# Optimization experiments

Measured on AMD Instinct MI355X. Metric: run time of the kernel, lower is better.

Reference implementation:

```python
import jax, jax.numpy as jnp
import numpy as np

B, NPG, K, C, IN_DIM, GS_DIM, NBLK, NCLF = 8, 12500, 128, 128, 7, 11, 4, 5
N = B * NPG          # 100000 total nodes
E = N * 8            # 800000 nnz in block-diagonal complex gradient operator


def setup_inputs() -> dict:
    key = jax.random.key(0)
    ks = jax.random.split(key, 20)
    x = jax.random.normal(ks[0], (N, IN_DIM), jnp.float32)
    evals = jax.random.uniform(ks[1], (B, K), jnp.float32) * 10.0  # nonneg eigenvalues
    evecs = jax.random.normal(ks[2], (N, K), jnp.float32) / np.float32(np.sqrt(NPG))
    mass = jax.random.uniform(ks[3], (N,), jnp.float32) + 0.1      # positive lumped mass
    graph_stats = jax.random.normal(ks[4], (B, GS_DIM), jnp.float32)
    batch = jnp.repeat(jnp.arange(B, dtype=jnp.int32), NPG)        # sorted graph ids
    epg = E // B
    offs = jnp.repeat(jnp.arange(B, dtype=jnp.int32) * NPG, epg)   # block-diagonal structure
    grad_rows = jax.random.randint(ks[5], (E,), 0, NPG, jnp.int32) + offs
    grad_cols = jax.random.randint(ks[6], (E,), 0, NPG, jnp.int32) + offs
    grad_vals_re = jax.random.normal(ks[7], (E,), jnp.float32) * 0.1
    grad_vals_im = jax.random.normal(ks[8], (E,), jnp.float32) * 0.1
    grad_n = jnp.full((B,), NPG, jnp.int32)
    s = lambda k, sh, fan: jax.random.normal(k, sh, jnp.float32) / np.float32(np.sqrt(fan))
    W_embed = s(ks[9], (IN_DIM, C), IN_DIM); b_embed = jnp.zeros((C,), jnp.float32)
    t_diff = jax.random.uniform(ks[10], (NBLK, C), jnp.float32) * 0.5 + 1e-3
    A_grad = s(ks[11], (NBLK, C, C), C)
    W1 = s(ks[12], (NBLK, 3 * C, C), 3 * C); b1 = jnp.zeros((NBLK, C), jnp.float32)
    W2 = s(ks[13], (NBLK, C, C), C);         b2 = jnp.zeros((NBLK, C), jnp.float32)
    Wh1 = s(ks[14], (C + GS_DIM, 64), C + GS_DIM); bh1 = jnp.zeros((64,), jnp.float32)
    Wh2 = s(ks[15], (64, NCLF), 64);               bh2 = jnp.zeros((NCLF,), jnp.float32)
    return dict(x=x, evals=evals, evecs=evecs, mass=mass, graph_stats=graph_stats,
                batch=batch, grad_rows=grad_rows, grad_cols=grad_cols,
                grad_vals_re=grad_vals_re, grad_vals_im=grad_vals_im, grad_n=grad_n,
                W_embed=W_embed, b_embed=b_embed, t_diff=t_diff, A_grad=A_grad,
                W1=W1, b1=b1, W2=W2, b2=b2, Wh1=Wh1, bh1=bh1, Wh2=Wh2, bh2=bh2)


def _forward(x, evals, evecs, mass, graph_stats, batch, grad_rows, grad_cols,
             vre, vim, W_embed, b_embed, t_diff, A_grad, W1, b1, W2, b2,
             Wh1, bh1, Wh2, bh2):
    n = x.shape[0]
    ev_r = evecs.reshape(B, NPG, K)              # per-graph spectral basis (equal-size graphs)
    h = jax.nn.relu(x @ W_embed + b_embed)       # embed: [N, C]
    for blk in range(NBLK):                      # fixed small number of blocks
        # --- learned-time spectral diffusion ---
        time = jnp.clip(jnp.abs(t_diff[blk]), 1e-8)            # [C]
        hm = (h * mass[:, None]).reshape(B, NPG, C)
        spec = jnp.einsum('bnk,bnc->bkc', ev_r, hm)            # to_basis: [B, K, C]
        spec = spec * jnp.exp(-evals[:, :, None] * time[None, None, :])
        h_diff = jnp.einsum('bnk,bkc->bnc', ev_r, spec).reshape(n, C)
        # --- block-sparse complex gradient: g = (vre + i*vim) @ h_diff ---
        xg = h_diff[grad_cols]                                 # [E, C] gather
        g_re = jnp.zeros((n, C), h.dtype).at[grad_rows].add(vre[:, None] * xg)
        g_im = jnp.zeros((n, C), h.dtype).at[grad_rows].add(vim[:, None] * xg)
        # --- spatial gradient features: tanh(Re(conj(g) * (A g))) ---
        A = A_grad[blk]
        g_feat = jnp.tanh(g_re * (g_re @ A.T) + g_im * (g_im @ A.T))
        # --- per-vertex MLP + residual (dropout = eval-mode identity) ---
        comb = jnp.concatenate([h, h_diff, g_feat], axis=-1)   # [N, 3C]
        h = h + (jax.nn.relu(comb @ W1[blk] + b1[blk]) @ W2[blk] + b2[blk])
    # --- fuse per-node features with gathered graph stats, node clf head ---
    fused = jnp.concatenate([h, graph_stats[batch]], axis=-1)  # [N, C+11]
    return jax.nn.relu(fused @ Wh1 + bh1) @ Wh2 + bh2          # [N, 5]


def reference(x, evals, evecs, mass, graph_stats, batch, grad_rows, grad_cols,
              grad_vals_re, grad_vals_im, grad_n, W_embed, b_embed, t_diff,
              A_grad, W1, b1, W2, b2, Wh1, bh1, Wh2, bh2):
    # Vectorized replacement of the original per-batch .item() nnz-count loop
    # (histogram of edge rows into per-graph node-offset bins); the block-sparse
    # operator is applied directly with global COO indices so nnz is only a stat.
    node_off = jnp.concatenate([jnp.zeros((1,), jnp.int32),
                                jnp.cumsum(grad_n)[:-1].astype(jnp.int32)])
    _grad_nnz = jnp.bincount(jnp.searchsorted(node_off, grad_rows, side='right') - 1, length=B)
    return _forward(x, evals, evecs, mass, graph_stats, batch, grad_rows, grad_cols,
                    grad_vals_re, grad_vals_im, W_embed, b_embed, t_diff, A_grad,
                    W1, b1, W2, b2, Wh1, bh1, Wh2, bh2)
```

## Files before the change

kernel.cpp:

```cpp
#include <hip/hip_runtime.h>
#include <hip/hip_bf16.h>

#define NNODES 100000
#define NPG    12500
#define NGRAPH 8
#define KD     128
#define CD     128
#define INDIM  7
#define GSDIM  11
#define NBLKS  4
#define NCLF   5
#define NEDGE  800000
#define BCAP   32
#define NPGP   12800
#define TBSPLIT 40
#define TBCHUNK 320
#define NT32    391
#define NT128   98

typedef __attribute__((ext_vector_type(8))) short short8v;
typedef __attribute__((ext_vector_type(4))) float f32x4;
typedef unsigned short u16;
typedef unsigned long long u64;

#define MFMA(acc, a, b) acc = __builtin_amdgcn_mfma_f32_16x16x32_bf16(a, b, acc, 0, 0, 0)

__device__ __forceinline__ u16 f2b(float f) {
  union { __hip_bfloat16 h; u16 u; } cv;
  cv.h = __float2bfloat16(f);
  return cv.u;
}
__device__ __forceinline__ float b2f(u16 u) {
  return __uint_as_float((unsigned)u << 16);
}


__device__ __forceinline__ void stage64_f32(u16* S, const float* src, int ld, int k0, int valid) {
  int t = threadIdx.x, row = t >> 2, kq = t & 3;
  alignas(16) u16 tmp[8] = {0, 0, 0, 0, 0, 0, 0, 0};
  if (row < valid) {
    const float* p = src + (size_t)row * ld + k0 + kq * 8;
    float4 f0 = *(const float4*)p, f1 = *(const float4*)(p + 4);
    tmp[0] = f2b(f0.x); tmp[1] = f2b(f0.y); tmp[2] = f2b(f0.z); tmp[3] = f2b(f0.w);
    tmp[4] = f2b(f1.x); tmp[5] = f2b(f1.y); tmp[6] = f2b(f1.z); tmp[7] = f2b(f1.w);
  }
  *(uint4*)&S[row * 40 + kq * 8] = *(uint4*)tmp;
}

__device__ __forceinline__ void stage64_b16(u16* S, const u16* src, long ld, int k0, int valid) {
  int t = threadIdx.x, row = t >> 2, kq = t & 3;
  uint4 v = make_uint4(0, 0, 0, 0);
  if (row < valid) v = *(const uint4*)(src + (size_t)row * ld + k0 + kq * 8);
  *(uint4*)&S[row * 40 + kq * 8] = v;
}

__device__ __forceinline__ void stage32_b16(u16* S, const u16* src, long ld, int k0, int valid) {
  int t = threadIdx.x;
  if (t < 128) {
    int row = t >> 2, kq = t & 3;
    uint4 v = make_uint4(0, 0, 0, 0);
    if (row < valid) v = *(const uint4*)(src + (size_t)row * ld + k0 + kq * 8);
    *(uint4*)&S[row * 40 + kq * 8] = v;
  }
}

__device__ __forceinline__ void stage128_b16(u16* S, const u16* src, long ld, int k0) {
  int t = threadIdx.x, row = t >> 1, half = t & 1;
  const u16* p = src + (size_t)row * ld + k0 + half * 16;
  uint4 v0 = *(const uint4*)p, v1 = *(const uint4*)(p + 8);
  *(uint4*)&S[row * 40 + half * 16] = v0;
  *(uint4*)&S[row * 40 + half * 16 + 8] = v1;
}

__device__ __forceinline__ void stage128_f32(u16* S, const float* src, int ld, int k0) {
  int t = threadIdx.x, row = t >> 1, half = t & 1;
  const float* p = src + (size_t)row * ld + k0 + half * 16;
  float4 f0 = *(const float4*)p, f1 = *(const float4*)(p + 4);
  float4 f2 = *(const float4*)(p + 8), f3 = *(const float4*)(p + 12);
  alignas(16) u16 tmp[16];
  tmp[0] = f2b(f0.x); tmp[1] = f2b(f0.y); tmp[2]  = f2b(f0.z); tmp[3]  = f2b(f0.w);
  tmp[4] = f2b(f1.x); tmp[5] = f2b(f1.y); tmp[6]  = f2b(f1.z); tmp[7]  = f2b(f1.w);
  tmp[8] = f2b(f2.x); tmp[9] = f2b(f2.y); tmp[10] = f2b(f2.z); tmp[11] = f2b(f2.w);
  tmp[12] = f2b(f3.x); tmp[13] = f2b(f3.y); tmp[14] = f2b(f3.z); tmp[15] = f2b(f3.w);
  *(uint4*)&S[row * 40 + half * 16] = *(uint4*)&tmp[0];
  *(uint4*)&S[row * 40 + half * 16 + 8] = *(uint4*)&tmp[8];
}

__device__ __forceinline__ void stageA_b16(u16* Af, const u16* src, long ld, int valid) {
  int t = threadIdx.x;
#pragma unroll
  for (int q = 0; q < 4; ++q) {
    int lin = t + q * 512;
    int row = lin >> 4, kq = lin & 15;
    uint4 v = make_uint4(0, 0, 0, 0);
    if (row < valid) v = *(const uint4*)(src + (size_t)row * ld + kq * 8);
    *(uint4*)&Af[row * 136 + kq * 8] = v;
  }
}
__device__ __forceinline__ void stageA_f32(u16* Af, const float* src, long ld, int valid) {
  int t = threadIdx.x;
#pragma unroll
  for (int q = 0; q < 4; ++q) {
    int lin = t + q * 512;
    int row = lin >> 4, kq = lin & 15;
    alignas(16) u16 tmp[8] = {0, 0, 0, 0, 0, 0, 0, 0};
    if (row < valid) {
      const float* p = src + (size_t)row * ld + kq * 8;
      float4 f0 = *(const float4*)p, f1 = *(const float4*)(p + 4);
      tmp[0] = f2b(f0.x); tmp[1] = f2b(f0.y); tmp[2] = f2b(f0.z); tmp[3] = f2b(f0.w);
      tmp[4] = f2b(f1.x); tmp[5] = f2b(f1.y); tmp[6] = f2b(f1.z); tmp[7] = f2b(f1.w);
    }
    *(uint4*)&Af[row * 136 + kq * 8] = *(uint4*)tmp;
  }
}

__device__ __forceinline__ uint4 ldB(const u16* bt, int k0) {
  int t = threadIdx.x, row = t >> 2, kq = t & 3;
  return *(const uint4*)(bt + (size_t)row * 128 + k0 + kq * 8);
}
__device__ __forceinline__ void stB(u16* Bs, uint4 v) {
  int t = threadIdx.x, row = t >> 2, kq = t & 3;
  *(uint4*)&Bs[row * 40 + kq * 8] = v;
}

__device__ __forceinline__ short8v frag(const u16* S, int row0, int l) {
  return *(const short8v*)&S[(row0 + (l & 15)) * 40 + (l >> 4) * 8];
}
__device__ __forceinline__ short8v frag_p(const u16* S, int row0, int l, int pitch, int k0) {
  return *(const short8v*)&S[(row0 + (l & 15)) * pitch + k0 + (l >> 4) * 8];
}


__global__ void k_fill0(float4* p, int n4) {
  int i = blockIdx.x * blockDim.x + threadIdx.x;
  int s = gridDim.x * blockDim.x;
  float4 z = make_float4(0.f, 0.f, 0.f, 0.f);
  for (; i < n4; i += s) p[i] = z;
}

__global__ __launch_bounds__(256) void k_embed2(const float* __restrict__ x,
                                                const float* __restrict__ W,
                                                const float* __restrict__ bv,
                                                const float* __restrict__ mass,
                                                u16* __restrict__ h16,
                                                u16* __restrict__ hmT) {
  int b = blockIdx.x / 200, tile = blockIdx.x % 200;
  int n0 = tile * 64;
  size_t gbase = (size_t)b * NPG;
  int t = threadIdx.x;
  __shared__ float xs[64][8];
  __shared__ float Ws[INDIM][128];
  __shared__ float bs[128];
  __shared__ float ms[64];
  __shared__ float ld[64][132];
  if (t < 128) bs[t] = bv[t];
  for (int i = t; i < INDIM * 128; i += 256) Ws[i >> 7][i & 127] = W[i];
  for (int i = t; i < 64 * INDIM; i += 256) {
    int r = i / INDIM, q = i % INDIM;
    int gn = n0 + r;
    xs[r][q] = (gn < NPG) ? x[(gbase + gn) * INDIM + q] : 0.f;
  }
  if (t < 64) {
    int gn = n0 + t;
    ms[t] = (gn < NPG) ? mass[gbase + gn] : 0.f;
  }
  __syncthreads();
  {
    int row = t & 63, c0 = (t >> 6) * 32;
#pragma unroll
    for (int cc = 0; cc < 32; ++cc) {
      int c = c0 + cc;
      float acc = bs[c];
#pragma unroll
      for (int i = 0; i < INDIM; ++i) acc = fmaf(xs[row][i], Ws[i][c], acc);
      ld[row][c] = fmaxf(acc, 0.f);
    }
  }
  __syncthreads();
  {
    int row = t >> 2, q = t & 3;
    if (n0 + row < NPG) {
      size_t base = (gbase + n0 + row) * (size_t)CD + q * 32;
      alignas(16) u16 tmp[8];
#pragma unroll
      for (int u = 0; u < 4; ++u) {
#pragma unroll
        for (int i = 0; i < 8; ++i) tmp[i] = f2b(ld[row][q * 32 + u * 8 + i]);
        *(uint4*)&h16[base + u * 8] = *(uint4*)tmp;
      }
    }
  }
  {
    int crow = t >> 1, half = t & 1;
    alignas(16) u16 tmp[8];
#pragma unroll
    for (int q = 0; q < 4; ++q) {
      int nb = half * 32 + q * 8;
#pragma unroll
      for (int i = 0; i < 8; ++i) tmp[i] = f2b(ld[nb + i][crow] * ms[nb + i]);
      *(uint4*)&hmT[((size_t)(b * 128 + crow)) * NPGP + n0 + nb] = *(uint4*)tmp;
    }
  }
}

__global__ void k_bucket_place(const int* __restrict__ rows, const int* __restrict__ cols,
                               const float* __restrict__ vre, const float* __restrict__ vim,
                               int* cnt, u64* bucket) {
  int e = blockIdx.x * 256 + threadIdx.x;
  if (e >= NEDGE) return;
  int r = rows[e];
  int pos = atomicAdd(&cnt[r], 1);
  if (pos < BCAP) {
    u64 ent = (u64)(unsigned)cols[e]
            | ((u64)f2b(vre[e]) << 32)
            | ((u64)f2b(vim[e]) << 48);
    bucket[(size_t)r * BCAP + pos] = ent;
  }
}

__global__ void k_gather_ev(const int* __restrict__ cnt, const u64* __restrict__ bucket,
                            const float* __restrict__ evf, const u16* __restrict__ ev16,
                            int useB16,
                            u16* __restrict__ gre, u16* __restrict__ gim) {
  int orig = blockIdx.x;
  int blk  = (orig & 7) * 3125 + (orig >> 3);
  int wv = threadIdx.x >> 6;
  int ln = threadIdx.x & 63;
  int r  = blk * 4 + wv;
  int d = min(cnt[r], BCAP);
  const u64* bk = bucket + (size_t)r * BCAP;
  float2 ra0 = make_float2(0.f, 0.f), ia0 = make_float2(0.f, 0.f);
  float2 ra1 = make_float2(0.f, 0.f), ia1 = make_float2(0.f, 0.f);
  if (useB16) {
    int i = 0;
    for (; i + 2 <= d; i += 2) {
      u64 e0 = bk[i], e1 = bk[i + 1];
      int c0 = (int)(unsigned)e0, c1 = (int)(unsigned)e1;
      float a0 = b2f((u16)(e0 >> 32)), b0 = b2f((u16)(e0 >> 48));
      float a1 = b2f((u16)(e1 >> 32)), b1 = b2f((u16)(e1 >> 48));
      ushort2 u0 = *(const ushort2*)&ev16[(size_t)c0 * KD + ln * 2];
      ushort2 u1 = *(const ushort2*)&ev16[(size_t)c1 * KD + ln * 2];
      float vx0 = b2f(u0.x), vy0 = b2f(u0.y);
      float vx1 = b2f(u1.x), vy1 = b2f(u1.y);
      ra0.x = fmaf(a0, vx0, ra0.x); ra0.y = fmaf(a0, vy0, ra0.y);
      ia0.x = fmaf(b0, vx0, ia0.x); ia0.y = fmaf(b0, vy0, ia0.y);
      ra1.x = fmaf(a1, vx1, ra1.x); ra1.y = fmaf(a1, vy1, ra1.y);
      ia1.x = fmaf(b1, vx1, ia1.x); ia1.y = fmaf(b1, vy1, ia1.y);
    }
    if (i < d) {
      u64 e0 = bk[i];
      int c0 = (int)(unsigned)e0;
      float a0 = b2f((u16)(e0 >> 32)), b0 = b2f((u16)(e0 >> 48));
      ushort2 u0 = *(const ushort2*)&ev16[(size_t)c0 * KD + ln * 2];
      float vx0 = b2f(u0.x), vy0 = b2f(u0.y);
      ra0.x = fmaf(a0, vx0, ra0.x); ra0.y = fmaf(a0, vy0, ra0.y);
      ia0.x = fmaf(b0, vx0, ia0.x); ia0.y = fmaf(b0, vy0, ia0.y);
    }
  } else {
    for (int i = 0; i < d; ++i) {
      u64 e0 = bk[i];
      int c0 = (int)(unsigned)e0;
      float a = b2f((u16)(e0 >> 32)), b = b2f((u16)(e0 >> 48));
      float2 v = *(const float2*)&evf[(size_t)c0 * KD + ln * 2];
      ra0.x = fmaf(a, v.x, ra0.x); ra0.y = fmaf(a, v.y, ra0.y);
      ia0.x = fmaf(b, v.x, ia0.x); ia0.y = fmaf(b, v.y, ia0.y);
    }
  }
  ushort2 ro, io;
  ro.x = f2b(ra0.x + ra1.x); ro.y = f2b(ra0.y + ra1.y);
  io.x = f2b(ia0.x + ia1.x); io.y = f2b(ia0.y + ia1.y);
  *(ushort2*)&gre[(size_t)r * KD + ln * 2] = ro;
  *(ushort2*)&gim[(size_t)r * KD + ln * 2] = io;
}

__global__ void k_prep_w(const float* __restrict__ W1, const float* __restrict__ W2,
                         u16* W1aT, u16* W1bT, u16* W1cT, u16* W2T) {
  int idx = blockIdx.x * 256 + threadIdx.x;
  int blk = idx >> 16, rem = idx & 65535;
  int mat = rem >> 14, e = rem & 16383;
  int j = e >> 7, c = e & 127;
  float v;
  u16* dst;
  if (mat < 3) {
    v = W1[(size_t)blk * 3 * 16384 + (size_t)mat * 16384 + e];
    dst = (mat == 0) ? W1aT : (mat == 1 ? W1bT : W1cT);
  } else {
    v = W2[(size_t)blk * 16384 + e];
    dst = W2T;
  }
  dst[(size_t)blk * 16384 + c * 128 + j] = f2b(v);
}

__global__ void k_prep_head(const float* __restrict__ Wh1, const float* __restrict__ Wh2,
                            u16* __restrict__ B1T, u16* __restrict__ B2T) {
  for (int idx = threadIdx.x; idx < 64 * 160; idx += 256) {
    int c = idx / 160, k = idx % 160;
    B1T[idx] = f2b(k < (CD + GSDIM) ? Wh1[k * 64 + c] : 0.f);
  }
  for (int idx = threadIdx.x; idx < 16 * 64; idx += 256) {
    int c = idx >> 6, k = idx & 63;
    B2T[idx] = f2b(c < NCLF ? Wh2[k * NCLF + c] : 0.f);
  }
}

__global__ void k_transpose_nk(const float* __restrict__ src, u16* __restrict__ dst,
                               u16* __restrict__ ev16, int writeMir) {
  int b = blockIdx.x / 200, tile = blockIdx.x % 200;
  int n0 = tile * 64;
  size_t gbase = (size_t)b * NPG;
  int t = threadIdx.x;
  __shared__ float ld[64][132];
  int row0 = t >> 5, c4 = t & 31;
#pragma unroll
  for (int it = 0; it < 8; ++it) {
    int r = it * 8 + row0;
    int gn = n0 + r;
    float4 v = make_float4(0.f, 0.f, 0.f, 0.f);
    if (gn < NPG) v = *(const float4*)&src[(gbase + gn) * KD + c4 * 4];
    *(float4*)&ld[r][c4 * 4] = v;
    if (writeMir && gn < NPG) {
      ushort4 o;
      o.x = f2b(v.x); o.y = f2b(v.y); o.z = f2b(v.z); o.w = f2b(v.w);
      *(ushort4*)&ev16[(gbase + gn) * KD + c4 * 4] = o;
    }
  }
  __syncthreads();
  int crow = t >> 1, half = t & 1;
  alignas(16) u16 tmp[8];
#pragma unroll
  for (int q = 0; q < 4; ++q) {
    int nb = half * 32 + q * 8;
#pragma unroll
    for (int i = 0; i < 8; ++i) tmp[i] = f2b(ld[nb + i][crow]);
    *(uint4*)&dst[((size_t)(b * 128 + crow)) * NPGP + n0 + nb] = *(uint4*)tmp;
  }
}


__global__ __launch_bounds__(256) void k_tobasis(const u16* __restrict__ evT,
                                                 const u16* __restrict__ hmT,
                                                 float* __restrict__ partials) {
  int g = blockIdx.x;
  int kt = g & 1;
  int s  = (g >> 1) % TBSPLIT;
  int b  = g / (2 * TBSPLIT);
  int t = threadIdx.x, w = t >> 6, l = t & 63;
  __shared__ u16 As[64 * 40];
  __shared__ u16 Bs[128 * 40];
  f32x4 acc[8];
  f32x4 z = {0.f, 0.f, 0.f, 0.f};
#pragma unroll
  for (int j = 0; j < 8; ++j) acc[j] = z;
  const u16* ae = evT + ((size_t)(b * 128 + kt * 64)) * NPGP + s * TBCHUNK;
  const u16* bh = hmT + (size_t)b * 128 * NPGP + s * TBCHUNK;
  for (int ks = 0; ks < TBCHUNK / 32; ++ks) {
    stage64_b16(As, ae, NPGP, ks * 32, 64);
    stage128_b16(Bs, bh, NPGP, ks * 32);
    __syncthreads();
    short8v a = frag(As, w * 16, l);
    __builtin_amdgcn_s_setprio(1);
#pragma unroll
    for (int j = 0; j < 8; ++j) MFMA(acc[j], a, frag(Bs, j * 16, l));
    __builtin_amdgcn_s_setprio(0);
    __syncthreads();
  }
  float* op = partials + (size_t)(b * TBSPLIT + s) * 16384 + kt * 64 * 128;
#pragma unroll
  for (int j = 0; j < 8; ++j)
#pragma unroll
    for (int i = 0; i < 4; ++i) {
      int krow = w * 16 + (l >> 4) * 4 + i;
      int c = j * 16 + (l & 15);
      op[krow * 128 + c] = acc[j][i];
    }
}

__global__ void k_reduce_scale_t(const float* __restrict__ partials,
                                 const float* __restrict__ evals,
                                 const float* __restrict__ td,
                                 float* __restrict__ spec, u16* __restrict__ specT) {
  int b = blockIdx.x >> 6;
  int idx = (blockIdx.x & 63) * 256 + threadIdx.x;
  int k = idx >> 7, c = idx & 127;
  float s = 0.f;
#pragma unroll 8
  for (int sp = 0; sp < TBSPLIT; ++sp)
    s += partials[(size_t)(b * TBSPLIT + sp) * 16384 + idx];
  float tm = fmaxf(fabsf(td[c]), 1e-8f);
  s *= expf(-evals[b * KD + k] * tm);
  spec[(size_t)b * 16384 + idx] = s;
  specT[(size_t)b * 16384 + c * 128 + k] = f2b(s);
}

__global__ __launch_bounds__(256) void k_smallT(const float* __restrict__ Agrad_blk,
                                                const u16* __restrict__ W1bT_blk,
                                                const float* __restrict__ spec,
                                                u16* __restrict__ SAT, u16* __restrict__ M1T) {
  int b = blockIdx.x & 7;
  int job = (blockIdx.x >> 3) & 1;
  int q = blockIdx.x >> 4;
  int t = threadIdx.x, w = t >> 6, l = t & 63;
  __shared__ u16 As[128 * 40];
  __shared__ u16 Bs[128 * 40];
  f32x4 acc[2][2];
  f32x4 z = {0.f, 0.f, 0.f, 0.f};
#pragma unroll
  for (int mi = 0; mi < 2; ++mi) { acc[mi][0] = z; acc[mi][1] = z; }
  for (int ks = 0; ks < 4; ++ks) {
    if (job == 0) stage128_f32(As, Agrad_blk, 128, ks * 32);
    else          stage128_b16(As, W1bT_blk, 128, ks * 32);
    stage128_f32(Bs, spec + (size_t)b * 16384, 128, ks * 32);
    __syncthreads();
    short8v a0 = frag(As, q * 32, l);
    short8v a1 = frag(As, q * 32 + 16, l);
#pragma unroll
    for (int jj = 0; jj < 2; ++jj) {
      short8v bj = frag(Bs, (w * 2 + jj) * 16, l);
      MFMA(acc[0][jj], a0, bj);
      MFMA(acc[1][jj], a1, bj);
    }
    __syncthreads();
  }
  u16* out = (job == 0 ? SAT : M1T) + (size_t)b * 16384;
#pragma unroll
  for (int mi = 0; mi < 2; ++mi)
#pragma unroll
    for (int jj = 0; jj < 2; ++jj)
#pragma unroll
      for (int i = 0; i < 4; ++i)
        out[(q * 32 + mi * 16 + (l >> 4) * 4 + i) * 128 + (w * 2 + jj) * 16 + (l & 15)] =
            f2b(acc[mi][jj][i]);
}

__global__ __launch_bounds__(256) void k_gfeat(const u16* __restrict__ Gre,
                                               const u16* __restrict__ Gim,
                                               const u16* __restrict__ specT,
                                               const u16* __restrict__ SAT,
                                               u16* __restrict__ gf) {
  int b = blockIdx.x / NT32, tile = blockIdx.x % NT32;
  int n0 = tile * 32;
  size_t gbase = (size_t)b * NPG;
  int t = threadIdx.x, w = t >> 6, l = t & 63;
  int r0 = (w & 1) * 16, c0 = (w >> 1) * 64;
  __shared__ u16 Sr[32 * 40];
  __shared__ u16 Si[32 * 40];
  __shared__ u16 Bs[128 * 40];
  __shared__ u16 Ba[128 * 40];
  f32x4 aGR[4], aAR[4], aGI[4], aAI[4];
  f32x4 z = {0.f, 0.f, 0.f, 0.f};
#pragma unroll
  for (int j = 0; j < 4; ++j) { aGR[j] = z; aAR[j] = z; aGI[j] = z; aAI[j] = z; }
  int valid = min(32, NPG - n0);
  const u16* gre = Gre + (gbase + n0) * KD;
  const u16* gim = Gim + (gbase + n0) * KD;
  for (int ks = 0; ks < 4; ++ks) {
    stage32_b16(Sr, gre, KD, ks * 32, valid);
    stage32_b16(Si, gim, KD, ks * 32, valid);
    stage128_b16(Bs, specT + (size_t)b * 16384, 128, ks * 32);
    stage128_b16(Ba, SAT + (size_t)b * 16384, 128, ks * 32);
    __syncthreads();
    short8v fr = frag(Sr, r0, l);
    short8v fi = frag(Si, r0, l);
    __builtin_amdgcn_s_setprio(1);
#pragma unroll
    for (int j = 0; j < 4; ++j) {
      short8v bs = frag(Bs, c0 + j * 16, l);
      short8v ba = frag(Ba, c0 + j * 16, l);
      MFMA(aGR[j], fr, bs);
      MFMA(aAR[j], fr, ba);
      MFMA(aGI[j], fi, bs);
      MFMA(aAI[j], fi, ba);
    }
    __builtin_amdgcn_s_setprio(0);
    __syncthreads();
  }
#pragma unroll
  for (int j = 0; j < 4; ++j) {
    int c = c0 + j * 16 + (l & 15);
#pragma unroll
    for (int i = 0; i < 4; ++i) {
      int n = n0 + r0 + (l >> 4) * 4 + i;
      if (n - n0 < valid) {
        float v = tanhf(fmaf(aGR[j][i], aAR[j][i], aGI[j][i] * aAI[j][i]));
        gf[(gbase + n) * CD + c] = f2b(v);
      }
    }
  }
}

__global__ __launch_bounds__(512) void k_mlp12(const float* __restrict__ evf,
                                               const u16* __restrict__ ev16,
                                               int useB16,
                                               const u16* __restrict__ gf,
                                               const u16* __restrict__ W1aT,
                                               const u16* __restrict__ M1T,
                                               const u16* __restrict__ W1cT,
                                               const float* __restrict__ b1,
                                               const u16* __restrict__ W2T,
                                               const float* __restrict__ b2,
                                               const float* __restrict__ mass,
                                               u16* __restrict__ h16,
                                               u16* __restrict__ hmT,
                                               int writeHmT) {
  int b = blockIdx.x / NT128, tile = blockIdx.x % NT128;
  int n0 = tile * 128;
  size_t gbase = (size_t)b * NPG;
  int t = threadIdx.x, w = t >> 6, l = t & 63;
  __shared__ u16 SH[27648];
  u16* Af  = SH;
  u16* t1S = SH;
  u16* Tm  = SH;
  u16* Bs0 = SH + 17408;
  u16* Bs1 = SH + 22528;
  f32x4 acc[8];
  f32x4 z = {0.f, 0.f, 0.f, 0.f};
#pragma unroll
  for (int j = 0; j < 8; ++j) acc[j] = z;
  int valid = min(128, NPG - n0);
  int r0 = w * 16;

  for (int seg = 0; seg < 3; ++seg) {
    const u16* bt = (seg == 0) ? W1aT : (seg == 1 ? M1T + (size_t)b * 16384 : W1cT);
    if (seg == 0)      stageA_b16(Af, h16 + (gbase + n0) * CD, CD, valid);
    else if (seg == 1) {
      if (useB16) stageA_b16(Af, ev16 + (gbase + n0) * KD, KD, valid);
      else        stageA_f32(Af, evf + (gbase + n0) * KD, KD, valid);
    }
    else               stageA_b16(Af, gf + (gbase + n0) * CD, CD, valid);
    stB(Bs0, ldB(bt, 0));
    __syncthreads();
#pragma unroll
    for (int ks = 0; ks < 4; ++ks) {
      uint4 bvn;
      if (ks < 3) bvn = ldB(bt, (ks + 1) * 32);
      short8v a = frag_p(Af, r0, l, 136, ks * 32);
      u16* Bcur = (ks & 1) ? Bs1 : Bs0;
      __builtin_amdgcn_s_setprio(1);
#pragma unroll
      for (int j = 0; j < 8; ++j) MFMA(acc[j], a, frag(Bcur, j * 16, l));
      __builtin_amdgcn_s_setprio(0);
      if (ks < 3) stB((ks & 1) ? Bs0 : Bs1, bvn);
      __syncthreads();
    }
  }
#pragma unroll
  for (int j = 0; j < 8; ++j) {
    int c = j * 16 + (l & 15);
    float bias = b1[c];
#pragma unroll
    for (int i = 0; i < 4; ++i) {
      int row = r0 + (l >> 4) * 4 + i;
      t1S[row * 132 + c] = f2b(fmaxf(acc[j][i] + bias, 0.f));
    }
  }
  stB(Bs0, ldB(W2T, 0));
  __syncthreads();

#pragma unroll
  for (int j = 0; j < 8; ++j) acc[j] = z;
#pragma unroll
  for (int ks = 0; ks < 4; ++ks) {
    uint4 bvn;
    if (ks < 3) bvn = ldB(W2T, (ks + 1) * 32);
    short8v a = frag_p(t1S, r0, l, 132, ks * 32);
    u16* Bcur = (ks & 1) ? Bs1 : Bs0;
    __builtin_amdgcn_s_setprio(1);
#pragma unroll
    for (int j = 0; j < 8; ++j) MFMA(acc[j], a, frag(Bcur, j * 16, l));
    __builtin_amdgcn_s_setprio(0);
    if (ks < 3) stB((ks & 1) ? Bs0 : Bs1, bvn);
    __syncthreads();
  }

  float massv[4];
#pragma unroll
  for (int i = 0; i < 4; ++i) {
    int nl = r0 + (l >> 4) * 4 + i;
    massv[i] = (nl < valid) ? mass[gbase + n0 + nl] : 0.f;
  }
#pragma unroll
  for (int j = 0; j < 8; ++j) {
    int c = j * 16 + (l & 15);
    float bias = b2[c];
#pragma unroll
    for (int i = 0; i < 4; ++i) {
      int nl = r0 + (l >> 4) * 4 + i;
      float hv = 0.f;
      if (nl < valid) {
        size_t idx = (gbase + n0 + nl) * (size_t)CD + c;
        hv = b2f(h16[idx]) + acc[j][i] + bias;
        h16[idx] = f2b(hv);
      }
      if (writeHmT) Tm[c * 130 + nl] = f2b(hv * massv[i]);
    }
  }
  if (writeHmT) {
    __syncthreads();
#pragma unroll
    for (int q = 0; q < 4; ++q) {
      int lin = t + q * 512;
      int cc = lin >> 4, chunk = lin & 15;
      *(uint4*)&hmT[((size_t)(b * 128 + cc)) * NPGP + n0 + chunk * 8] =
          *(const uint4*)&Tm[cc * 130 + chunk * 8];
    }
  }
}

__global__ __launch_bounds__(256) void k_head2(
    const u16* __restrict__ h16, const float* __restrict__ gs,
    const int* __restrict__ batch, const u16* __restrict__ B1T,
    const float* __restrict__ bh1, const u16* __restrict__ B2T,
    const float* __restrict__ bh2, float* __restrict__ out) {
  int n0 = blockIdx.x * 64;
  int t = threadIdx.x, w = t >> 6, l = t & 63;
  __shared__ u16 As[64 * 40];
  __shared__ u16 Bs[64 * 40];
  __shared__ u16 zS[64 * 72];
  int valid = min(64, NNODES - n0);
  f32x4 acc1[4];
  f32x4 z = {0.f, 0.f, 0.f, 0.f};
#pragma unroll
  for (int j = 0; j < 4; ++j) acc1[j] = z;
  for (int ks = 0; ks < 5; ++ks) {
    if (ks < 4) {
      stage64_b16(As, h16 + (size_t)n0 * CD, CD, ks * 32, valid);
    } else {
      int row = t >> 2, kq = t & 3;
      alignas(16) u16 tmp[8];
      int bb = (row < valid) ? batch[n0 + row] : 0;
#pragma unroll
      for (int q = 0; q < 8; ++q) {
        int kk = kq * 8 + q;
        float v = (row < valid && kk < GSDIM) ? gs[bb * GSDIM + kk] : 0.f;
        tmp[q] = f2b(v);
      }
      *(uint4*)&As[row * 40 + kq * 8] = *(uint4*)tmp;
    }
    stage64_b16(Bs, B1T, 160, ks * 32, 64);
    __syncthreads();
    short8v a = frag(As, w * 16, l);
#pragma unroll
    for (int j = 0; j < 4; ++j) MFMA(acc1[j], a, frag(Bs, j * 16, l));
    __syncthreads();
  }
#pragma unroll
  for (int j = 0; j < 4; ++j) {
    int c = j * 16 + (l & 15);
    float bias = bh1[c];
#pragma unroll
    for (int i = 0; i < 4; ++i) {
      int row = w * 16 + (l >> 4) * 4 + i;
      zS[row * 72 + c] = f2b(fmaxf(acc1[j][i] + bias, 0.f));
    }
  }
  __syncthreads();
  f32x4 acc2 = z;
  for (int ks = 0; ks < 2; ++ks) {
    stage64_b16(Bs, B2T, 64, ks * 32, 16);
    __syncthreads();
    short8v a2 = frag_p(zS, w * 16, l, 72, ks * 32);
    MFMA(acc2, a2, frag(Bs, 0, l));
    __syncthreads();
  }
  int c = l & 15;
  if (c < NCLF) {
    float bias = bh2[c];
#pragma unroll
    for (int i = 0; i < 4; ++i) {
      int n = n0 + w * 16 + (l >> 4) * 4 + i;
      if (n < NNODES) out[(size_t)n * NCLF + c] = acc2[i] + bias;
    }
  }
}

extern "C" void kernel_launch(void* const* d_in, const int* in_sizes, int n_in,
                              void* d_out, int out_size, void* d_ws, size_t ws_size,
                              hipStream_t stream) {
  const float* x     = (const float*)d_in[0];
  const float* evals = (const float*)d_in[1];
  const float* evecs = (const float*)d_in[2];
  const float* mass  = (const float*)d_in[3];
  const float* gs    = (const float*)d_in[4];
  const int*   batch = (const int*)d_in[5];
  const int*   grows = (const int*)d_in[6];
  const int*   gcols = (const int*)d_in[7];
  const float* vre   = (const float*)d_in[8];
  const float* vim   = (const float*)d_in[9];
  const float* Wemb  = (const float*)d_in[11];
  const float* bemb  = (const float*)d_in[12];
  const float* tdiff = (const float*)d_in[13];
  const float* Agrad = (const float*)d_in[14];
  const float* W1    = (const float*)d_in[15];
  const float* b1    = (const float*)d_in[16];
  const float* W2    = (const float*)d_in[17];
  const float* b2    = (const float*)d_in[18];
  const float* Wh1   = (const float*)d_in[19];
  const float* bh1   = (const float*)d_in[20];
  const float* Wh2   = (const float*)d_in[21];
  const float* bh2   = (const float*)d_in[22];

  char* base = (char*)d_ws;
  size_t off = 0;
  auto alloc = [&](size_t bytes) -> void* {
    void* p = base + off;
    off += (bytes + 255) & ~(size_t)255;
    return p;
  };
  u16*   evT16  = (u16*)alloc((size_t)NGRAPH * 128 * NPGP * 2);
  u16*   hmT    = (u16*)alloc((size_t)NGRAPH * 128 * NPGP * 2);
  u16*   Gre16  = (u16*)alloc((size_t)NNODES * KD * 2);
  u16*   Gim16  = (u16*)alloc((size_t)NNODES * KD * 2);
  u16*   h16    = (u16*)alloc((size_t)NNODES * CD * 2);
  float* spec   = (float*)alloc((size_t)NGRAPH * 16384 * 4);
  u16*   specT16 = (u16*)alloc((size_t)NGRAPH * 16384 * 2);
  u16*   SAT16  = (u16*)alloc((size_t)NGRAPH * 16384 * 2);
  u16*   M1T16  = (u16*)alloc((size_t)NGRAPH * 16384 * 2);
  u16*   W1aT16 = (u16*)alloc((size_t)NBLKS * 16384 * 2);
  u16*   W1bT16 = (u16*)alloc((size_t)NBLKS * 16384 * 2);
  u16*   W1cT16 = (u16*)alloc((size_t)NBLKS * 16384 * 2);
  u16*   W2T16  = (u16*)alloc((size_t)NBLKS * 16384 * 2);
  u16*   B1T16  = (u16*)alloc(64 * 160 * 2);
  u16*   B2T16  = (u16*)alloc(16 * 64 * 2);
  int*   cnt    = (int*)alloc(100352 * 4);
  void*  R      = alloc((size_t)NNODES * BCAP * 8);
  u64*   bucket = (u64*)R;
  float* partials = (float*)R;
  u16*   gf16   = (u16*)R;
  int useEv16 = 0;
  u16* ev16 = nullptr;
  if (off + ((size_t)NNODES * KD * 2 + 256) <= ws_size) {
    ev16 = (u16*)alloc((size_t)NNODES * KD * 2);
    useEv16 = 1;
  }
  float* out    = (float*)d_out;

  k_embed2<<<NGRAPH * 200, 256, 0, stream>>>(x, Wemb, bemb, mass, h16, hmT);
  k_fill0<<<98, 256, 0, stream>>>((float4*)cnt, 100352 / 4);
  k_bucket_place<<<(NEDGE + 255) / 256, 256, 0, stream>>>(grows, gcols, vre, vim,
                                                          cnt, bucket);
  k_transpose_nk<<<NGRAPH * 200, 256, 0, stream>>>(evecs, evT16, ev16, useEv16);
  k_gather_ev<<<NNODES / 4, 256, 0, stream>>>(cnt, bucket, evecs, ev16, useEv16,
                                              Gre16, Gim16);
  k_prep_w<<<1024, 256, 0, stream>>>(W1, W2, W1aT16, W1bT16, W1cT16, W2T16);
  k_prep_head<<<1, 256, 0, stream>>>(Wh1, Wh2, B1T16, B2T16);

  for (int blk = 0; blk < NBLKS; ++blk) {
    k_tobasis<<<NGRAPH * TBSPLIT * 2, 256, 0, stream>>>(evT16, hmT, partials);
    k_reduce_scale_t<<<NGRAPH * 64, 256, 0, stream>>>(partials, evals, tdiff + blk * CD,
                                                      spec, specT16);
    k_smallT<<<64, 256, 0, stream>>>(Agrad + (size_t)blk * 16384,
                                     W1bT16 + (size_t)blk * 16384, spec, SAT16, M1T16);
    k_gfeat<<<NGRAPH * NT32, 256, 0, stream>>>(Gre16, Gim16, specT16, SAT16, gf16);
    k_mlp12<<<NGRAPH * NT128, 512, 0, stream>>>(evecs, ev16, useEv16, gf16,
                                                W1aT16 + (size_t)blk * 16384, M1T16,
                                                W1cT16 + (size_t)blk * 16384,
                                                b1 + blk * CD,
                                                W2T16 + (size_t)blk * 16384,
                                                b2 + blk * CD, mass, h16, hmT,
                                                (blk < NBLKS - 1) ? 1 : 0);
  }
  k_head2<<<(NNODES + 63) / 64, 256, 0, stream>>>(h16, gs, batch, B1T16, bh1,
                                                  B2T16, bh2, out);
}
```

Measured before the change: 647.0 us.

## Fold mass into transposed evecs and compute full 128x128 tile per tobasis block

The mass weighting moves from the per-block hidden transpose (embed and mlp12 epilogues) into the one-time evecs transpose, so the hidden transpose is stored unweighted and the per-block mass loads go away. k_tobasis now computes both 64-row k halves in one workgroup with two accumulator sets, sharing each staged B tile across twice the MFMAs. The number of tobasis blocks is halved, which improves B-tile reuse at the cost of more registers per thread and fewer blocks to fill the GPU.

```diff
diff --git a/kernel.cpp b/kernel.cpp
--- a/kernel.cpp
+++ b/kernel.cpp
@@ -141,9 +141,8 @@
 __global__ __launch_bounds__(256) void k_embed2(const float* __restrict__ x,
                                                 const float* __restrict__ W,
                                                 const float* __restrict__ bv,
-                                                const float* __restrict__ mass,
                                                 u16* __restrict__ h16,
-                                                u16* __restrict__ hmT) {
+                                                u16* __restrict__ hT) {
   int b = blockIdx.x / 200, tile = blockIdx.x % 200;
   int n0 = tile * 64;
   size_t gbase = (size_t)b * NPG;
@@ -151,7 +150,6 @@
   __shared__ float xs[64][8];
   __shared__ float Ws[INDIM][128];
   __shared__ float bs[128];
-  __shared__ float ms[64];
   __shared__ float ld[64][132];
   if (t < 128) bs[t] = bv[t];
   for (int i = t; i < INDIM * 128; i += 256) Ws[i >> 7][i & 127] = W[i];
@@ -160,10 +158,6 @@
     int gn = n0 + r;
     xs[r][q] = (gn < NPG) ? x[(gbase + gn) * INDIM + q] : 0.f;
   }
-  if (t < 64) {
-    int gn = n0 + t;
-    ms[t] = (gn < NPG) ? mass[gbase + gn] : 0.f;
-  }
   __syncthreads();
   {
     int row = t & 63, c0 = (t >> 6) * 32;
@@ -197,8 +191,8 @@
     for (int q = 0; q < 4; ++q) {
       int nb = half * 32 + q * 8;
 #pragma unroll
-      for (int i = 0; i < 8; ++i) tmp[i] = f2b(ld[nb + i][crow] * ms[nb + i]);
-      *(uint4*)&hmT[((size_t)(b * 128 + crow)) * NPGP + n0 + nb] = *(uint4*)tmp;
+      for (int i = 0; i < 8; ++i) tmp[i] = f2b(ld[nb + i][crow]);
+      *(uint4*)&hT[((size_t)(b * 128 + crow)) * NPGP + n0 + nb] = *(uint4*)tmp;
     }
   }
 }
@@ -303,13 +297,18 @@
   }
 }
 
-__global__ void k_transpose_nk(const float* __restrict__ src, u16* __restrict__ dst,
-                               u16* __restrict__ ev16, int writeMir) {
+__global__ void k_transpose_nk(const float* __restrict__ src, const float* __restrict__ mass,
+                               u16* __restrict__ dst, u16* __restrict__ ev16, int writeMir) {
   int b = blockIdx.x / 200, tile = blockIdx.x % 200;
   int n0 = tile * 64;
   size_t gbase = (size_t)b * NPG;
   int t = threadIdx.x;
   __shared__ float ld[64][132];
+  __shared__ float ms[64];
+  if (t < 64) {
+    int gn = n0 + t;
+    ms[t] = (gn < NPG) ? mass[gbase + gn] : 0.f;
+  }
   int row0 = t >> 5, c4 = t & 31;
 #pragma unroll
   for (int it = 0; it < 8; ++it) {
@@ -331,48 +330,55 @@
   for (int q = 0; q < 4; ++q) {
     int nb = half * 32 + q * 8;
 #pragma unroll
-    for (int i = 0; i < 8; ++i) tmp[i] = f2b(ld[nb + i][crow]);
+    for (int i = 0; i < 8; ++i) tmp[i] = f2b(ld[nb + i][crow] * ms[nb + i]);
     *(uint4*)&dst[((size_t)(b * 128 + crow)) * NPGP + n0 + nb] = *(uint4*)tmp;
   }
 }
 
 
-__global__ __launch_bounds__(256) void k_tobasis(const u16* __restrict__ evT,
-                                                 const u16* __restrict__ hmT,
+__global__ __launch_bounds__(256) void k_tobasis(const u16* __restrict__ evTm,
+                                                 const u16* __restrict__ hT,
                                                  float* __restrict__ partials) {
-  int g = blockIdx.x;
-  int kt = g & 1;
-  int s  = (g >> 1) % TBSPLIT;
-  int b  = g / (2 * TBSPLIT);
+  int s = blockIdx.x % TBSPLIT;
+  int b = blockIdx.x / TBSPLIT;
   int t = threadIdx.x, w = t >> 6, l = t & 63;
-  __shared__ u16 As[64 * 40];
+  __shared__ u16 As[128 * 40];
   __shared__ u16 Bs[128 * 40];
-  f32x4 acc[8];
+  f32x4 acc[2][8];
   f32x4 z = {0.f, 0.f, 0.f, 0.f};
 #pragma unroll
-  for (int j = 0; j < 8; ++j) acc[j] = z;
-  const u16* ae = evT + ((size_t)(b * 128 + kt * 64)) * NPGP + s * TBCHUNK;
-  const u16* bh = hmT + (size_t)b * 128 * NPGP + s * TBCHUNK;
+  for (int mi = 0; mi < 2; ++mi)
+#pragma unroll
+    for (int j = 0; j < 8; ++j) acc[mi][j] = z;
+  const u16* ae = evTm + (size_t)b * 128 * NPGP + s * TBCHUNK;
+  const u16* bh = hT   + (size_t)b * 128 * NPGP + s * TBCHUNK;
   for (int ks = 0; ks < TBCHUNK / 32; ++ks) {
-    stage64_b16(As, ae, NPGP, ks * 32, 64);
+    stage128_b16(As, ae, NPGP, ks * 32);
     stage128_b16(Bs, bh, NPGP, ks * 32);
     __syncthreads();
-    short8v a = frag(As, w * 16, l);
+    short8v a0 = frag(As, w * 32, l);
+    short8v a1 = frag(As, w * 32 + 16, l);
     __builtin_amdgcn_s_setprio(1);
 #pragma unroll
-    for (int j = 0; j < 8; ++j) MFMA(acc[j], a, frag(Bs, j * 16, l));
+    for (int j = 0; j < 8; ++j) {
+      short8v bj = frag(Bs, j * 16, l);
+      MFMA(acc[0][j], a0, bj);
+      MFMA(acc[1][j], a1, bj);
+    }
     __builtin_amdgcn_s_setprio(0);
     __syncthreads();
   }
-  float* op = partials + (size_t)(b * TBSPLIT + s) * 16384 + kt * 64 * 128;
-#pragma unroll
-  for (int j = 0; j < 8; ++j)
-#pragma unroll
-    for (int i = 0; i < 4; ++i) {
-      int krow = w * 16 + (l >> 4) * 4 + i;
-      int c = j * 16 + (l & 15);
-      op[krow * 128 + c] = acc[j][i];
-    }
+  float* op = partials + (size_t)(b * TBSPLIT + s) * 16384;
+#pragma unroll
+  for (int mi = 0; mi < 2; ++mi)
+#pragma unroll
+    for (int j = 0; j < 8; ++j)
+#pragma unroll
+      for (int i = 0; i < 4; ++i) {
+        int krow = w * 32 + mi * 16 + (l >> 4) * 4 + i;
+        int c = j * 16 + (l & 15);
+        op[krow * 128 + c] = acc[mi][j][i];
+      }
 }
 
 __global__ void k_reduce_scale_t(const float* __restrict__ partials,
@@ -498,10 +504,9 @@
                                                const float* __restrict__ b1,
                                                const u16* __restrict__ W2T,
                                                const float* __restrict__ b2,
-                                               const float* __restrict__ mass,
                                                u16* __restrict__ h16,
-                                               u16* __restrict__ hmT,
-                                               int writeHmT) {
+                                               u16* __restrict__ hT,
+                                               int writeHT) {
   int b = blockIdx.x / NT128, tile = blockIdx.x % NT128;
   int n0 = tile * 128;
   size_t gbase = (size_t)b * NPG;
@@ -572,12 +577,6 @@
     __syncthreads();
   }
 
-  float massv[4];
-#pragma unroll
-  for (int i = 0; i < 4; ++i) {
-    int nl = r0 + (l >> 4) * 4 + i;
-    massv[i] = (nl < valid) ? mass[gbase + n0 + nl] : 0.f;
-  }
 #pragma unroll
   for (int j = 0; j < 8; ++j) {
     int c = j * 16 + (l & 15);
@@ -591,16 +590,16 @@
         hv = b2f(h16[idx]) + acc[j][i] + bias;
         h16[idx] = f2b(hv);
       }
-      if (writeHmT) Tm[c * 130 + nl] = f2b(hv * massv[i]);
-    }
-  }
-  if (writeHmT) {
+      if (writeHT) Tm[c * 130 + nl] = f2b(hv);
+    }
+  }
+  if (writeHT) {
     __syncthreads();
 #pragma unroll
     for (int q = 0; q < 4; ++q) {
       int lin = t + q * 512;
       int cc = lin >> 4, chunk = lin & 15;
-      *(uint4*)&hmT[((size_t)(b * 128 + cc)) * NPGP + n0 + chunk * 8] =
+      *(uint4*)&hT[((size_t)(b * 128 + cc)) * NPGP + n0 + chunk * 8] =
           *(const uint4*)&Tm[cc * 130 + chunk * 8];
     }
   }
@@ -707,7 +706,7 @@
     return p;
   };
   u16*   evT16  = (u16*)alloc((size_t)NGRAPH * 128 * NPGP * 2);
-  u16*   hmT    = (u16*)alloc((size_t)NGRAPH * 128 * NPGP * 2);
+  u16*   hT     = (u16*)alloc((size_t)NGRAPH * 128 * NPGP * 2);
   u16*   Gre16  = (u16*)alloc((size_t)NNODES * KD * 2);
   u16*   Gim16  = (u16*)alloc((size_t)NNODES * KD * 2);
   u16*   h16    = (u16*)alloc((size_t)NNODES * CD * 2);
@@ -734,18 +733,18 @@
   }
   float* out    = (float*)d_out;
 
-  k_embed2<<<NGRAPH * 200, 256, 0, stream>>>(x, Wemb, bemb, mass, h16, hmT);
+  k_embed2<<<NGRAPH * 200, 256, 0, stream>>>(x, Wemb, bemb, h16, hT);
   k_fill0<<<98, 256, 0, stream>>>((float4*)cnt, 100352 / 4);
   k_bucket_place<<<(NEDGE + 255) / 256, 256, 0, stream>>>(grows, gcols, vre, vim,
                                                           cnt, bucket);
-  k_transpose_nk<<<NGRAPH * 200, 256, 0, stream>>>(evecs, evT16, ev16, useEv16);
+  k_transpose_nk<<<NGRAPH * 200, 256, 0, stream>>>(evecs, mass, evT16, ev16, useEv16);
   k_gather_ev<<<NNODES / 4, 256, 0, stream>>>(cnt, bucket, evecs, ev16, useEv16,
                                               Gre16, Gim16);
   k_prep_w<<<1024, 256, 0, stream>>>(W1, W2, W1aT16, W1bT16, W1cT16, W2T16);
   k_prep_head<<<1, 256, 0, stream>>>(Wh1, Wh2, B1T16, B2T16);
 
   for (int blk = 0; blk < NBLKS; ++blk) {
-    k_tobasis<<<NGRAPH * TBSPLIT * 2, 256, 0, stream>>>(evT16, hmT, partials);
+    k_tobasis<<<NGRAPH * TBSPLIT, 256, 0, stream>>>(evT16, hT, partials);
     k_reduce_scale_t<<<NGRAPH * 64, 256, 0, stream>>>(partials, evals, tdiff + blk * CD,
                                                       spec, specT16);
     k_smallT<<<64, 256, 0, stream>>>(Agrad + (size_t)blk * 16384,
@@ -756,7 +755,7 @@
                                                 W1cT16 + (size_t)blk * 16384,
                                                 b1 + blk * CD,
                                                 W2T16 + (size_t)blk * 16384,
-                                                b2 + blk * CD, mass, h16, hmT,
+                                                b2 + blk * CD, h16, hT,
                                                 (blk < NBLKS - 1) ? 1 : 0);
   }
   k_head2<<<(NNODES + 63) / 64, 256, 0, stream>>>(h16, gs, batch, B1T16, bh1,
```

Result: no change. 640.2 us (-1.0%).
